# Kernel tuning notes

Measured on AMD Instinct MI355X. Metric: run time of the kernel, lower is better.

The kernel has to match this reference:

```python
import jax, jax.numpy as jnp
import numpy as np

B, N, C = 4, 4096, 384
D = H3 = W3 = 16          # input_size
WS = 8                    # window_size (divides 16 -> no padding)
NH = 6                    # num_heads
HD = C // NH              # head_dim = 64


def setup_inputs() -> dict:
    key = jax.random.key(0)
    ks = jax.random.split(key, 8)
    return {
        "x": jax.random.normal(ks[0], (B, N, C), jnp.float32),
        "qkv_w": jax.random.normal(ks[1], (C, 3 * C), jnp.float32) * 0.02,
        "qkv_b": jax.random.normal(ks[2], (3 * C,), jnp.float32) * 0.02,
        "proj_w": jax.random.normal(ks[3], (C, C), jnp.float32) * 0.02,
        "proj_b": jax.random.normal(ks[4], (C,), jnp.float32) * 0.02,
        "rel_pos_x": jax.random.normal(ks[5], (2 * WS - 1, HD), jnp.float32) * 0.02,
        "rel_pos_y": jax.random.normal(ks[6], (2 * WS - 1, HD), jnp.float32) * 0.02,
        "rel_pos_z": jax.random.normal(ks[7], (2 * WS - 1, HD), jnp.float32) * 0.02,
    }


def reference(x, qkv_w, qkv_b, proj_w, proj_b, rel_pos_x, rel_pos_y, rel_pos_z):
    nd = D // WS                      # windows per spatial dim = 2
    b_ = B * nd * nd * nd             # 32 windows
    T = WS * WS * WS                  # 512 tokens per window
    scale = HD ** -0.5

    # window partition: [B,N,C] -> [b_, T, C]
    x3 = x.reshape(B, nd, WS, nd, WS, nd, WS, C)
    x3 = x3.transpose(0, 1, 3, 5, 2, 4, 6, 7)
    xf = x3.reshape(b_, T, C)

    # qkv projection
    qkv = xf @ qkv_w + qkv_b                                  # [b_, T, 3C]
    qkv = qkv.reshape(b_, T, 3, NH, HD).transpose(2, 0, 3, 1, 4)
    q, k, v = qkv[0], qkv[1], qkv[2]                          # [b_, NH, T, HD]

    attn = jnp.einsum('bhqc,bhkc->bhqk', q * scale, k)        # [b_, NH, T, T]

    # decomposed 3D relative position bias (q_size == k_size == WS)
    coords = jnp.arange(WS)[:, None] - jnp.arange(WS)[None, :] + (WS - 1)
    Rx = rel_pos_x[coords]                                    # [WS, WS, HD]
    Ry = rel_pos_y[coords]
    Rz = rel_pos_z[coords]
    rq = q.reshape(b_ * NH, WS, WS, WS, HD)
    rel_x = jnp.einsum('bdhwc,dkc->bdhwk', rq, Rx)
    rel_y = jnp.einsum('bdhwc,hkc->bdhwk', rq, Ry)
    rel_z = jnp.einsum('bdhwc,wkc->bdhwk', rq, Rz)
    a = attn.reshape(b_ * NH, WS, WS, WS, WS, WS, WS)
    a = (a + rel_x[:, :, :, :, :, None, None]
           + rel_y[:, :, :, :, None, :, None]
           + rel_z[:, :, :, :, None, None, :])
    attn = a.reshape(b_, NH, T, T)

    attn = jax.nn.softmax(attn, axis=-1)
    out = jnp.einsum('bhqk,bhkc->bhqc', attn, v)              # [b_, NH, T, HD]
    out = out.transpose(0, 2, 1, 3).reshape(b_, T, C)
    out = out @ proj_w + proj_b

    # window unpartition: [b_, T, C] -> [B, N, C]
    o = out.reshape(B, nd, nd, nd, WS, WS, WS, C)
    o = o.transpose(0, 1, 4, 2, 5, 3, 6, 7).reshape(B, D, H3, W3, C)
    return o.reshape(B, N, C)
```

## Files before the change

kernel.cpp:

```cpp
#include <hip/hip_runtime.h>
#include <hip/hip_bf16.h>

typedef __bf16 bf16_t;
typedef __bf16 bf16x8 __attribute__((ext_vector_type(8)));
typedef __bf16 bf16x4 __attribute__((ext_vector_type(4)));
typedef float f32x4 __attribute__((ext_vector_type(4)));

#define MFMA16(a, b, c) __builtin_amdgcn_mfma_f32_16x16x32_bf16((a), (b), (c), 0, 0, 0)

__device__ __forceinline__ f32x4 v4zero() {
  f32x4 z = {0.f, 0.f, 0.f, 0.f};
  return z;
}

__device__ __forceinline__ int xrow_of(int m) {
  int win = m >> 9, t = m & 511;
  int b = win >> 3, d1 = (win >> 2) & 1, h1 = (win >> 1) & 1, w1 = win & 1;
  int d2 = t >> 6, h2 = (t >> 3) & 7, w2 = t & 7;
  return (b << 12) | ((d1 * 8 + d2) << 8) | ((h1 * 8 + h2) << 4) | (w1 * 8 + w2);
}

__global__ __launch_bounds__(256) void qkv_kernel(
    const float* __restrict__ x, const float* __restrict__ w,
    const float* __restrict__ bias, bf16_t* __restrict__ qg,
    bf16_t* __restrict__ kg, bf16_t* __restrict__ vtg) {
  __shared__ __align__(16) bf16_t At[128][40];
  __shared__ __align__(16) bf16_t Bt[128][40];
  const int tid = threadIdx.x;
  const int lane = tid & 63, wv = tid >> 6;
  const int m0 = blockIdx.x * 128, n0 = blockIdx.y * 128;

  const int arow = tid >> 1, aseg = tid & 1;
  const float* asrc = x + (size_t)xrow_of(m0 + arow) * 384 + aseg * 16;
  const int bn = tid & 127, bks = (tid >> 7) * 16;

  const int wr = (wv >> 1) * 64, wc = (wv & 1) * 64;
  const int lr = lane & 15, lk = (lane >> 4) * 8;

  f32x4 acc[4][4];
#pragma unroll
  for (int fr = 0; fr < 4; ++fr)
#pragma unroll
    for (int fc = 0; fc < 4; ++fc) acc[fr][fc] = v4zero();

  for (int kt = 0; kt < 12; ++kt) {
    f32x4 av0 = *(const f32x4*)(asrc + kt * 32);
    f32x4 av1 = *(const f32x4*)(asrc + kt * 32 + 4);
    f32x4 av2 = *(const f32x4*)(asrc + kt * 32 + 8);
    f32x4 av3 = *(const f32x4*)(asrc + kt * 32 + 12);
    bf16x8 a0, a1;
#pragma unroll
    for (int i = 0; i < 4; ++i) {
      a0[i] = (bf16_t)av0[i];
      a0[4 + i] = (bf16_t)av1[i];
      a1[i] = (bf16_t)av2[i];
      a1[4 + i] = (bf16_t)av3[i];
    }
    bf16x8 b0, b1;
#pragma unroll
    for (int i = 0; i < 8; ++i)
      b0[i] = (bf16_t)w[(size_t)(kt * 32 + bks + i) * 1152 + n0 + bn];
#pragma unroll
    for (int i = 0; i < 8; ++i)
      b1[i] = (bf16_t)w[(size_t)(kt * 32 + bks + 8 + i) * 1152 + n0 + bn];
    *(bf16x8*)&At[arow][aseg * 16] = a0;
    *(bf16x8*)&At[arow][aseg * 16 + 8] = a1;
    *(bf16x8*)&Bt[bn][bks] = b0;
    *(bf16x8*)&Bt[bn][bks + 8] = b1;
    __syncthreads();
    bf16x8 af[4], bfv[4];
#pragma unroll
    for (int fr = 0; fr < 4; ++fr) af[fr] = *(const bf16x8*)&At[wr + fr * 16 + lr][lk];
#pragma unroll
    for (int fc = 0; fc < 4; ++fc) bfv[fc] = *(const bf16x8*)&Bt[wc + fc * 16 + lr][lk];
#pragma unroll
    for (int fr = 0; fr < 4; ++fr)
#pragma unroll
      for (int fc = 0; fc < 4; ++fc)
        acc[fr][fc] = MFMA16(af[fr], bfv[fc], acc[fr][fc]);
    __syncthreads();
  }

  const int colb = n0 + wc;
  const int type = colb >= 768 ? 2 : (colb >= 384 ? 1 : 0);
#pragma unroll
  for (int fc = 0; fc < 4; ++fc) {
    const int col = colb + fc * 16 + lr;
    const float bc = bias[col];
    const int cc = col - type * 384;
    const int hh = cc >> 6, c = cc & 63;
#pragma unroll
    for (int fr = 0; fr < 4; ++fr) {
      const int m = m0 + wr + fr * 16 + (lane >> 4) * 4;
      const int win = m >> 9, t = m & 511;
      if (type == 2) {
        bf16x4 pk;
#pragma unroll
        for (int r = 0; r < 4; ++r) pk[r] = (bf16_t)(acc[fr][fc][r] + bc);
        *(bf16x4*)(vtg + ((size_t)(win * 6 + hh) * 64 + c) * 512 + t) = pk;
      } else {
        bf16_t* dst = (type == 0 ? qg : kg) + ((size_t)(win * 6 + hh) * 512 + t) * 64 + c;
#pragma unroll
        for (int r = 0; r < 4; ++r) dst[(size_t)r * 64] = (bf16_t)(acc[fr][fc][r] + bc);
      }
    }
  }
}

__global__ __launch_bounds__(256) void attn_kernel(
    const bf16_t* __restrict__ qg, const bf16_t* __restrict__ kg,
    const bf16_t* __restrict__ vtg, const float* __restrict__ rpx,
    const float* __restrict__ rpy, const float* __restrict__ rpz,
    bf16_t* __restrict__ ao) {
  __shared__ __align__(16) char smem[32768];
  __shared__ __align__(16) float rxT[8][132];
  const int tid = threadIdx.x, lane = tid & 63, wv = tid >> 6;
  const int hh = blockIdx.x, win = blockIdx.y, qt = blockIdx.z;
  const int wh = win * 6 + hh;
  const bf16_t* Qb = qg + (size_t)wh * 32768 + (size_t)qt * 8192;
  const bf16_t* Kb = kg + (size_t)wh * 32768;
  const bf16_t* Vb = vtg + (size_t)wh * 32768;

  bf16_t(*Qsh)[68] = (bf16_t(*)[68])smem;
  bf16_t(*Rsh)[68] = (bf16_t(*)[68])(smem + 17408);
  float(*Gsh)[132] = (float(*)[132])smem;
  bf16_t(*Ksh)[64][64] = (bf16_t(*)[64][64])smem;
  bf16_t(*Vsh)[64][64] = (bf16_t(*)[64][64])(smem + 16384);

  for (int i = tid; i < 1024; i += 256) {
    int row = i >> 3, slot = i & 7;
    *(bf16x8*)&Qsh[row][slot * 8] = *(const bf16x8*)(Qb + row * 64 + slot * 8);
  }
  for (int i = tid; i < 360; i += 256) {
    int row = i >> 3, slot = i & 7;
    int axis = row / 15, j = row - axis * 15;
    const float* RP = (axis == 0) ? rpx : (axis == 1) ? rpy : rpz;
    f32x4 r0 = *(const f32x4*)(RP + j * 64 + slot * 8);
    f32x4 r1 = *(const f32x4*)(RP + j * 64 + slot * 8 + 4);
    bf16x8 p;
#pragma unroll
    for (int jj = 0; jj < 4; ++jj) {
      p[jj] = (bf16_t)r0[jj];
      p[4 + jj] = (bf16_t)r1[jj];
    }
    *(bf16x8*)&Rsh[row][slot * 8] = p;
  }
  bf16x8 kreg[2], vreg[2];
#pragma unroll
  for (int r = 0; r < 2; ++r) {
    int ci = r * 256 + tid, row = ci >> 3, slot = ci & 7;
    kreg[r] = *(const bf16x8*)(Kb + (size_t)row * 64 + slot * 8);
    vreg[r] = *(const bf16x8*)(Vb + (size_t)row * 512 + slot * 8);
  }
  __syncthreads();

  const int lr = lane & 15, lg = lane >> 4;
  const int qrow0 = qt * 128 + wv * 32;
  const int qrb = wv * 32 + lr;

  bf16x8 bq[2][2];
#pragma unroll
  for (int fq = 0; fq < 2; ++fq)
#pragma unroll
    for (int ks = 0; ks < 2; ++ks)
      bq[fq][ks] = *(const bf16x8*)&Qsh[wv * 32 + fq * 16 + lr][ks * 32 + lg * 8];

  bf16x8 br[3][2];
#pragma unroll
  for (int jt = 0; jt < 3; ++jt)
#pragma unroll
    for (int ks = 0; ks < 2; ++ks)
      br[jt][ks] = *(const bf16x8*)&Rsh[jt * 16 + lr][ks * 32 + lg * 8];

  f32x4 gacc[2][3];
#pragma unroll
  for (int fq = 0; fq < 2; ++fq)
#pragma unroll
    for (int jt = 0; jt < 3; ++jt) {
      f32x4 g = MFMA16(bq[fq][0], br[jt][0], v4zero());
      gacc[fq][jt] = MFMA16(bq[fq][1], br[jt][1], g);
    }
  __syncthreads();

#pragma unroll
  for (int fq = 0; fq < 2; ++fq)
#pragma unroll
    for (int jt = 0; jt < 3; ++jt)
#pragma unroll
      for (int r = 0; r < 4; ++r)
        Gsh[jt * 16 + lr][(wv * 2 + fq) * 16 + lg * 4 + r] = gacc[fq][jt][r];
  __syncthreads();

  f32x4 byz[2][4];
#pragma unroll
  for (int fq = 0; fq < 2; ++fq) {
    const int q_r = qrb + fq * 16;
    const int qh_ = (q_r >> 3) & 7, qw_ = q_r & 7, qd_ = qt * 2 + (q_r >> 6);
#pragma unroll
    for (int fk = 0; fk < 4; ++fk) {
      f32x4 v;
#pragma unroll
      for (int i = 0; i < 4; ++i) {
        int kkl = fk * 16 + lg * 4 + i;
        v[i] = Gsh[15 + qh_ - (kkl >> 3) + 7][q_r] + Gsh[30 + qw_ - (kkl & 7) + 7][q_r];
      }
      byz[fq][fk] = v;
    }
    if (lg == 0) {
#pragma unroll
      for (int kt = 0; kt < 8; ++kt) rxT[kt][q_r] = Gsh[qd_ - kt + 7][q_r];
    }
  }
  __syncthreads();

#pragma unroll
  for (int r = 0; r < 2; ++r) {
    int ci = r * 256 + tid, row = ci >> 3, slot = ci & 7;
    *(bf16x8*)&Ksh[0][row][(slot ^ (row & 7)) * 8] = kreg[r];
    *(bf16x8*)&Vsh[0][row][(slot ^ (row & 7)) * 8] = vreg[r];
    kreg[r] = *(const bf16x8*)(Kb + (size_t)(64 + row) * 64 + slot * 8);
    vreg[r] = *(const bf16x8*)(Vb + (size_t)row * 512 + 64 + slot * 8);
  }
  __syncthreads();

  float rsum[2] = {0.f, 0.f};
  f32x4 oacc[2][4];
#pragma unroll
  for (int fq = 0; fq < 2; ++fq)
#pragma unroll
    for (int fc = 0; fc < 4; ++fc) oacc[fq][fc] = v4zero();

  for (int kt = 0; kt < 8; ++kt) {
    const int cur = kt & 1;
    bf16x8 ak[4][2];
#pragma unroll
    for (int fk = 0; fk < 4; ++fk) {
      const int row = fk * 16 + lr;
#pragma unroll
      for (int ks = 0; ks < 2; ++ks)
        ak[fk][ks] = *(const bf16x8*)&Ksh[cur][row][((ks * 4 + lg) ^ (row & 7)) * 8];
    }

    f32x4 sb[2][4];
#pragma unroll
    for (int fq = 0; fq < 2; ++fq) {
      const float rx = rxT[kt][qrb + fq * 16];
#pragma unroll
      for (int fk = 0; fk < 4; ++fk) {
        f32x4 s = MFMA16(ak[fk][0], bq[fq][0], v4zero());
        s = MFMA16(ak[fk][1], bq[fq][1], s);
        sb[fq][fk] = s * 0.125f + rx + byz[fq][fk];
      }
    }

#pragma unroll
    for (int fq = 0; fq < 2; ++fq) {
      float rs = 0.f;
#pragma unroll
      for (int fk = 0; fk < 4; ++fk)
#pragma unroll
        for (int i = 0; i < 4; ++i) {
          float p = __expf(sb[fq][fk][i]);
          sb[fq][fk][i] = p;
          rs += p;
        }
      rsum[fq] += rs;
    }

    bf16x8 pa[2][2];
#pragma unroll
    for (int fq = 0; fq < 2; ++fq)
#pragma unroll
      for (int h = 0; h < 2; ++h) {
#pragma unroll
        for (int j = 0; j < 4; ++j) {
          pa[fq][h][j] = (bf16_t)sb[fq][2 * h][j];
          pa[fq][h][4 + j] = (bf16_t)sb[fq][2 * h + 1][j];
        }
      }

#pragma unroll
    for (int h = 0; h < 2; ++h)
#pragma unroll
      for (int fc2 = 0; fc2 < 4; ++fc2) {
        const int row = fc2 * 16 + lr;
        const int c0 = (((h * 4 + (lg >> 1)) ^ (row & 7)) * 8) + (lg & 1) * 4;
        const int c1 = (((h * 4 + 2 + (lg >> 1)) ^ (row & 7)) * 8) + (lg & 1) * 4;
        bf16x4 v0 = *(const bf16x4*)&Vsh[cur][row][c0];
        bf16x4 v1 = *(const bf16x4*)&Vsh[cur][row][c1];
        bf16x8 bv;
#pragma unroll
        for (int j = 0; j < 4; ++j) {
          bv[j] = v0[j];
          bv[4 + j] = v1[j];
        }
#pragma unroll
        for (int fq = 0; fq < 2; ++fq)
          oacc[fq][fc2] = MFMA16(pa[fq][h], bv, oacc[fq][fc2]);
      }

    if (kt < 7) {
#pragma unroll
      for (int r = 0; r < 2; ++r) {
        int ci = r * 256 + tid, row = ci >> 3, slot = ci & 7;
        *(bf16x8*)&Ksh[cur ^ 1][row][(slot ^ (row & 7)) * 8] = kreg[r];
        *(bf16x8*)&Vsh[cur ^ 1][row][(slot ^ (row & 7)) * 8] = vreg[r];
        if (kt < 6) {
          kreg[r] = *(const bf16x8*)(Kb + (size_t)((kt + 2) * 64 + row) * 64 + slot * 8);
          vreg[r] = *(const bf16x8*)(Vb + (size_t)row * 512 + (kt + 2) * 64 + slot * 8);
        }
      }
    }
    __syncthreads();
  }

#pragma unroll
  for (int fq = 0; fq < 2; ++fq) {
    rsum[fq] += __shfl_xor(rsum[fq], 16);
    rsum[fq] += __shfl_xor(rsum[fq], 32);
  }
  f32x4 linv[2];
#pragma unroll
  for (int fq = 0; fq < 2; ++fq)
#pragma unroll
    for (int i = 0; i < 4; ++i)
      linv[fq][i] = 1.0f / __shfl(rsum[fq], lg * 4 + i);

#pragma unroll
  for (int fq = 0; fq < 2; ++fq)
#pragma unroll
    for (int fc2 = 0; fc2 < 4; ++fc2) {
      size_t base = ((size_t)win * 512 + qrow0 + fq * 16 + lg * 4) * 384 + hh * 64 + fc2 * 16 + lr;
#pragma unroll
      for (int i = 0; i < 4; ++i)
        ao[base + (size_t)i * 384] = (bf16_t)(oacc[fq][fc2][i] * linv[fq][i]);
    }
}

__global__ __launch_bounds__(256) void proj_kernel(
    const bf16_t* __restrict__ ain, const float* __restrict__ w,
    const float* __restrict__ bias, float* __restrict__ out) {
  __shared__ __align__(16) bf16_t At[128][40];
  __shared__ __align__(16) bf16_t Bt[128][40];
  const int tid = threadIdx.x;
  const int lane = tid & 63, wv = tid >> 6;
  const int m0 = blockIdx.x * 128, n0 = blockIdx.y * 128;

  const int arow = tid >> 1, aseg = tid & 1;
  const bf16_t* asrc = ain + (size_t)(m0 + arow) * 384 + aseg * 16;
  const int bn = tid & 127, bks = (tid >> 7) * 16;

  const int wr = (wv >> 1) * 64, wc = (wv & 1) * 64;
  const int lr = lane & 15, lk = (lane >> 4) * 8;

  f32x4 acc[4][4];
#pragma unroll
  for (int fr = 0; fr < 4; ++fr)
#pragma unroll
    for (int fc = 0; fc < 4; ++fc) acc[fr][fc] = v4zero();

  for (int kt = 0; kt < 12; ++kt) {
    bf16x8 a0 = *(const bf16x8*)(asrc + kt * 32);
    bf16x8 a1 = *(const bf16x8*)(asrc + kt * 32 + 8);
    bf16x8 b0, b1;
#pragma unroll
    for (int i = 0; i < 8; ++i)
      b0[i] = (bf16_t)w[(size_t)(kt * 32 + bks + i) * 384 + n0 + bn];
#pragma unroll
    for (int i = 0; i < 8; ++i)
      b1[i] = (bf16_t)w[(size_t)(kt * 32 + bks + 8 + i) * 384 + n0 + bn];
    *(bf16x8*)&At[arow][aseg * 16] = a0;
    *(bf16x8*)&At[arow][aseg * 16 + 8] = a1;
    *(bf16x8*)&Bt[bn][bks] = b0;
    *(bf16x8*)&Bt[bn][bks + 8] = b1;
    __syncthreads();
    bf16x8 af[4], bfv[4];
#pragma unroll
    for (int fr = 0; fr < 4; ++fr) af[fr] = *(const bf16x8*)&At[wr + fr * 16 + lr][lk];
#pragma unroll
    for (int fc = 0; fc < 4; ++fc) bfv[fc] = *(const bf16x8*)&Bt[wc + fc * 16 + lr][lk];
#pragma unroll
    for (int fr = 0; fr < 4; ++fr)
#pragma unroll
      for (int fc = 0; fc < 4; ++fc)
        acc[fr][fc] = MFMA16(af[fr], bfv[fc], acc[fr][fc]);
    __syncthreads();
  }

#pragma unroll
  for (int fc = 0; fc < 4; ++fc) {
    const int col = n0 + wc + fc * 16 + lr;
    const float bc = bias[col];
#pragma unroll
    for (int fr = 0; fr < 4; ++fr) {
      const int m = m0 + wr + fr * 16 + (lane >> 4) * 4;
#pragma unroll
      for (int r = 0; r < 4; ++r)
        out[(size_t)xrow_of(m + r) * 384 + col] = acc[fr][fc][r] + bc;
    }
  }
}

extern "C" void kernel_launch(void* const* d_in, const int* in_sizes, int n_in,
                              void* d_out, int out_size, void* d_ws, size_t ws_size,
                              hipStream_t stream) {
  (void)in_sizes; (void)n_in; (void)out_size;
  const float* x = (const float*)d_in[0];
  const float* qkv_w = (const float*)d_in[1];
  const float* qkv_b = (const float*)d_in[2];
  const float* proj_w = (const float*)d_in[3];
  const float* proj_b = (const float*)d_in[4];
  const float* rpx = (const float*)d_in[5];
  const float* rpy = (const float*)d_in[6];
  const float* rpz = (const float*)d_in[7];
  float* out = (float*)d_out;

  const size_t NE = 6291456;
  if (ws_size < NE * 4 * sizeof(bf16_t)) return;
  bf16_t* qg = (bf16_t*)d_ws;
  bf16_t* kg = qg + NE;
  bf16_t* vtg = kg + NE;
  bf16_t* ao = vtg + NE;

  qkv_kernel<<<dim3(128, 9), 256, 0, stream>>>(x, qkv_w, qkv_b, qg, kg, vtg);
  attn_kernel<<<dim3(6, 32, 4), 256, 0, stream>>>(qg, kg, vtg, rpx, rpy, rpz, ao);
  proj_kernel<<<dim3(128, 3), 256, 0, stream>>>(ao, proj_w, proj_b, out);
}
```

Baseline: 101.6 us.

## Double-buffer QKV GEMM tiles and stage Q/K epilogue through LDS for vector stores

The QKV projection kernel now double-buffers its LDS A/B tiles and prefetches global loads two k-steps ahead in registers, so global load latency overlaps the MFMA work and only one barrier runs per iteration. The Q/K epilogue writes the tile into shared memory first, then emits full 16-byte row stores instead of scattered 2-byte stores. This raises LDS use to 40 KB and register pressure, which may lower occupancy.

Measured after the change: 92.65 us. 8.8% less time.

```diff
diff --git a/kernel.cpp b/kernel.cpp
--- a/kernel.cpp
+++ b/kernel.cpp
@@ -24,8 +24,11 @@
     const float* __restrict__ x, const float* __restrict__ w,
     const float* __restrict__ bias, bf16_t* __restrict__ qg,
     bf16_t* __restrict__ kg, bf16_t* __restrict__ vtg) {
-  __shared__ __align__(16) bf16_t At[128][40];
-  __shared__ __align__(16) bf16_t Bt[128][40];
+  __shared__ __align__(16) char smem[40960];
+  bf16_t(*As)[128][40] = (bf16_t(*)[128][40])smem;
+  bf16_t(*Bs)[128][40] = (bf16_t(*)[128][40])(smem + 20480);
+  bf16_t(*Csh)[136] = (bf16_t(*)[136])smem;
+
   const int tid = threadIdx.x;
   const int lane = tid & 63, wv = tid >> 6;
   const int m0 = blockIdx.x * 128, n0 = blockIdx.y * 128;
@@ -33,9 +36,10 @@
   const int arow = tid >> 1, aseg = tid & 1;
   const float* asrc = x + (size_t)xrow_of(m0 + arow) * 384 + aseg * 16;
   const int bn = tid & 127, bks = (tid >> 7) * 16;
+  const float* bsrc = w + (size_t)bks * 1152 + n0 + bn;
 
   const int wr = (wv >> 1) * 64, wc = (wv & 1) * 64;
-  const int lr = lane & 15, lk = (lane >> 4) * 8;
+  const int lr = lane & 15, lg = lane >> 4, lk = lg * 8;
 
   f32x4 acc[4][4];
 #pragma unroll
@@ -43,67 +47,98 @@
 #pragma unroll
     for (int fc = 0; fc < 4; ++fc) acc[fr][fc] = v4zero();
 
+  f32x4 afr[4];
+  float bfr[16];
+
+#define LOAD_TILE(kt)                                              \
+  {                                                                \
+    _Pragma("unroll") for (int i = 0; i < 4; ++i)                  \
+        afr[i] = *(const f32x4*)(asrc + (kt)*32 + i * 4);          \
+    _Pragma("unroll") for (int i = 0; i < 16; ++i)                 \
+        bfr[i] = bsrc[(size_t)((kt)*32 + i) * 1152];               \
+  }
+
+#define STAGE_TILE(buf)                                            \
+  {                                                                \
+    bf16x8 a0, a1, b0, b1;                                         \
+    _Pragma("unroll") for (int i = 0; i < 4; ++i) {                \
+      a0[i] = (bf16_t)afr[0][i];                                   \
+      a0[4 + i] = (bf16_t)afr[1][i];                               \
+      a1[i] = (bf16_t)afr[2][i];                                   \
+      a1[4 + i] = (bf16_t)afr[3][i];                               \
+    }                                                              \
+    _Pragma("unroll") for (int i = 0; i < 8; ++i) {                \
+      b0[i] = (bf16_t)bfr[i];                                      \
+      b1[i] = (bf16_t)bfr[8 + i];                                  \
+    }                                                              \
+    *(bf16x8*)&As[buf][arow][aseg * 16] = a0;                      \
+    *(bf16x8*)&As[buf][arow][aseg * 16 + 8] = a1;                  \
+    *(bf16x8*)&Bs[buf][bn][bks] = b0;                              \
+    *(bf16x8*)&Bs[buf][bn][bks + 8] = b1;                          \
+  }
+
+  LOAD_TILE(0);
+  STAGE_TILE(0);
+  LOAD_TILE(1);
+  __syncthreads();
+
   for (int kt = 0; kt < 12; ++kt) {
-    f32x4 av0 = *(const f32x4*)(asrc + kt * 32);
-    f32x4 av1 = *(const f32x4*)(asrc + kt * 32 + 4);
-    f32x4 av2 = *(const f32x4*)(asrc + kt * 32 + 8);
-    f32x4 av3 = *(const f32x4*)(asrc + kt * 32 + 12);
-    bf16x8 a0, a1;
-#pragma unroll
-    for (int i = 0; i < 4; ++i) {
-      a0[i] = (bf16_t)av0[i];
-      a0[4 + i] = (bf16_t)av1[i];
-      a1[i] = (bf16_t)av2[i];
-      a1[4 + i] = (bf16_t)av3[i];
-    }
-    bf16x8 b0, b1;
-#pragma unroll
-    for (int i = 0; i < 8; ++i)
-      b0[i] = (bf16_t)w[(size_t)(kt * 32 + bks + i) * 1152 + n0 + bn];
-#pragma unroll
-    for (int i = 0; i < 8; ++i)
-      b1[i] = (bf16_t)w[(size_t)(kt * 32 + bks + 8 + i) * 1152 + n0 + bn];
-    *(bf16x8*)&At[arow][aseg * 16] = a0;
-    *(bf16x8*)&At[arow][aseg * 16 + 8] = a1;
-    *(bf16x8*)&Bt[bn][bks] = b0;
-    *(bf16x8*)&Bt[bn][bks + 8] = b1;
-    __syncthreads();
+    const int cur = kt & 1;
     bf16x8 af[4], bfv[4];
 #pragma unroll
-    for (int fr = 0; fr < 4; ++fr) af[fr] = *(const bf16x8*)&At[wr + fr * 16 + lr][lk];
-#pragma unroll
-    for (int fc = 0; fc < 4; ++fc) bfv[fc] = *(const bf16x8*)&Bt[wc + fc * 16 + lr][lk];
+    for (int fr = 0; fr < 4; ++fr) af[fr] = *(const bf16x8*)&As[cur][wr + fr * 16 + lr][lk];
+#pragma unroll
+    for (int fc = 0; fc < 4; ++fc) bfv[fc] = *(const bf16x8*)&Bs[cur][wc + fc * 16 + lr][lk];
 #pragma unroll
     for (int fr = 0; fr < 4; ++fr)
 #pragma unroll
       for (int fc = 0; fc < 4; ++fc)
         acc[fr][fc] = MFMA16(af[fr], bfv[fc], acc[fr][fc]);
+    if (kt < 11) {
+      STAGE_TILE(cur ^ 1);
+      if (kt < 10) LOAD_TILE(kt + 2);
+    }
     __syncthreads();
   }
-
-  const int colb = n0 + wc;
-  const int type = colb >= 768 ? 2 : (colb >= 384 ? 1 : 0);
-#pragma unroll
-  for (int fc = 0; fc < 4; ++fc) {
-    const int col = colb + fc * 16 + lr;
-    const float bc = bias[col];
-    const int cc = col - type * 384;
-    const int hh = cc >> 6, c = cc & 63;
-#pragma unroll
-    for (int fr = 0; fr < 4; ++fr) {
-      const int m = m0 + wr + fr * 16 + (lane >> 4) * 4;
-      const int win = m >> 9, t = m & 511;
-      if (type == 2) {
+#undef LOAD_TILE
+#undef STAGE_TILE
+
+  const int type = n0 / 384;
+  if (type == 2) {
+#pragma unroll
+    for (int fc = 0; fc < 4; ++fc) {
+      const int col = n0 + wc + fc * 16 + lr;
+      const float bc = bias[col];
+      const int cc = col - 768, hh = cc >> 6, c = cc & 63;
+#pragma unroll
+      for (int fr = 0; fr < 4; ++fr) {
+        const int m = m0 + wr + fr * 16 + lg * 4;
+        const int win = m >> 9, t = m & 511;
         bf16x4 pk;
 #pragma unroll
         for (int r = 0; r < 4; ++r) pk[r] = (bf16_t)(acc[fr][fc][r] + bc);
         *(bf16x4*)(vtg + ((size_t)(win * 6 + hh) * 64 + c) * 512 + t) = pk;
-      } else {
-        bf16_t* dst = (type == 0 ? qg : kg) + ((size_t)(win * 6 + hh) * 512 + t) * 64 + c;
-#pragma unroll
-        for (int r = 0; r < 4; ++r) dst[(size_t)r * 64] = (bf16_t)(acc[fr][fc][r] + bc);
-      }
-    }
+      }
+    }
+  } else {
+#pragma unroll
+    for (int fc = 0; fc < 4; ++fc) {
+      const int col = n0 + wc + fc * 16 + lr;
+      const float bc = bias[col];
+#pragma unroll
+      for (int fr = 0; fr < 4; ++fr)
+#pragma unroll
+        for (int r = 0; r < 4; ++r)
+          Csh[wr + fr * 16 + lg * 4 + r][wc + fc * 16 + lr] = (bf16_t)(acc[fr][fc][r] + bc);
+    }
+    __syncthreads();
+    const int mloc = tid >> 1, half = tid & 1;
+    const int hh2 = ((n0 - type * 384) >> 6) + half;
+    const int m = m0 + mloc, win = m >> 9, t = m & 511;
+    bf16_t* dst = (type == 0 ? qg : kg) + ((size_t)(win * 6 + hh2) * 512 + t) * 64;
+#pragma unroll
+    for (int j = 0; j < 8; ++j)
+      *(bf16x8*)(dst + j * 8) = *(const bf16x8*)&Csh[mloc][half * 64 + j * 8];
   }
 }
 
```
